# Performance work log

Measured on AMD Instinct MI355X. Metric: run time of the kernel, lower is better.

Reference implementation:

```python
import jax, jax.numpy as jnp
import numpy as np

N_IN = 200000
N_OUT = 600000
K = 27          # 3x3x3 kernel offsets
P = 150000      # kernel-map pairs per offset
C_IN = 96
C_OUT = 96
BN_EPS = 1e-5


def setup_inputs() -> dict:
    key = jax.random.key(0)
    k1, k2, k3, k4 = jax.random.split(key, 4)
    feats = jax.random.normal(k1, (N_IN, C_IN), dtype=jnp.float32)
    # kernel map: per offset, input-site indices and output-site indices
    in_idx = jax.random.randint(k2, (K, P), 0, N_IN, dtype=jnp.int32)
    out_idx = jax.random.randint(k3, (K, P), 0, N_OUT, dtype=jnp.int32)
    weight = jax.random.normal(k4, (K, C_IN, C_OUT), dtype=jnp.float32) * (1.0 / np.sqrt(C_IN * K))
    gamma = jnp.ones((C_OUT,), dtype=jnp.float32)
    beta = jnp.zeros((C_OUT,), dtype=jnp.float32)
    return {"feats": feats, "in_idx": in_idx, "out_idx": out_idx,
            "weight": weight, "gamma": gamma, "beta": beta}


def reference(feats, in_idx, out_idx, weight, gamma, beta):
    # Sparse transposed conv: gather -> matmul -> scatter-add per kernel offset.
    out = jnp.zeros((N_OUT, C_OUT), dtype=feats.dtype)
    for k in range(K):  # fixed small loop over kernel offsets (structurally distinct weights)
        contrib = feats[in_idx[k]] @ weight[k]          # [P, C_OUT]
        out = out.at[out_idx[k]].add(contrib)
    # BatchNorm (training-mode batch stats over active output sites), per channel
    mean = jnp.mean(out, axis=0)
    var = jnp.mean((out - mean) ** 2, axis=0)
    y = (out - mean) * jax.lax.rsqrt(var + BN_EPS) * gamma + beta
    # ReLU
    return jax.nn.relu(y)
```

## Files before the change

### kernel.cpp

```cpp
#include <hip/hip_runtime.h>
#include <hip/hip_bf16.h>

#define N_IN   200000
#define N_OUT  600000
#define KOFF   27
#define PPAIR  150000
#define NPAIR  (KOFF * PPAIR)
#define C      96
#define BN_EPS 1e-5f

using bf16x8 = __attribute__((ext_vector_type(8))) __bf16;
using f32x4  = __attribute__((ext_vector_type(4))) float;
using u32x2  = __attribute__((ext_vector_type(2))) unsigned int;
using u32x4  = __attribute__((ext_vector_type(4))) unsigned int;

static __device__ __forceinline__ unsigned short f2b(float x) {
    __hip_bfloat16 h = __float2bfloat16(x);
    return *reinterpret_cast<unsigned short*>(&h);
}
static __device__ __forceinline__ float b_lo(unsigned int u) { return __uint_as_float(u << 16); }
static __device__ __forceinline__ float b_hi(unsigned int u) { return __uint_as_float(u & 0xffff0000u); }

__global__ void cvt_feats(const float* __restrict__ src, unsigned short* __restrict__ dst) {
    int t = blockIdx.x * 256 + threadIdx.x;
    const float4* s4 = (const float4*)src;
    float4 a = s4[2 * t], b = s4[2 * t + 1];
    union { unsigned short u[8]; uint4 v; } r;
    r.u[0] = f2b(a.x); r.u[1] = f2b(a.y); r.u[2] = f2b(a.z); r.u[3] = f2b(a.w);
    r.u[4] = f2b(b.x); r.u[5] = f2b(b.y); r.u[6] = f2b(b.z); r.u[7] = f2b(b.w);
    ((uint4*)dst)[t] = r.v;
}

__global__ void cvt_w(const float* __restrict__ w, unsigned short* __restrict__ wt) {
    int t = blockIdx.x * 256 + threadIdx.x;
    int k = t / 9216;
    int rem = t - k * 9216;
    int o = rem / 96;
    int i = rem - o * 96;
    wt[t] = f2b(w[k * 9216 + i * 96 + o]);
}

__global__ void k_hist(const int* __restrict__ out_idx, int* __restrict__ counts,
                       unsigned char* __restrict__ lrank) {
    int t = blockIdx.x * 256 + threadIdx.x;
    if (t < NPAIR) lrank[t] = (unsigned char)atomicAdd(&counts[out_idx[t]], 1);
}

__global__ void k_bsum(const int* __restrict__ counts, int* __restrict__ bsum) {
    __shared__ int ls[256];
    int b = blockIdx.x, t = threadIdx.x;
    int base = b * 1024 + t * 4;
    int s = 0;
#pragma unroll
    for (int j = 0; j < 4; j++) { int i = base + j; if (i < N_OUT) s += counts[i]; }
    ls[t] = s;
    __syncthreads();
    for (int off = 128; off > 0; off >>= 1) {
        if (t < off) ls[t] += ls[t + off];
        __syncthreads();
    }
    if (t == 0) bsum[b] = ls[0];
}

__global__ void k_scan_bsum(const int* __restrict__ bsum, int* __restrict__ bsum_ex) {
    __shared__ int sc[1024];
    int t = threadIdx.x;
    int v = (t < 586) ? bsum[t] : 0;
    sc[t] = v;
    __syncthreads();
    for (int off = 1; off < 1024; off <<= 1) {
        int add = (t >= off) ? sc[t - off] : 0;
        __syncthreads();
        sc[t] += add;
        __syncthreads();
    }
    bsum_ex[t] = sc[t] - v;
}

__global__ void k_scan_local(int* __restrict__ csr, const int* __restrict__ bsum_ex) {
    __shared__ int sc[256];
    int b = blockIdx.x, t = threadIdx.x;
    int base = b * 1024 + t * 4;
    int c[4];
    int s = 0;
#pragma unroll
    for (int j = 0; j < 4; j++) {
        int i = base + j;
        c[j] = (i < N_OUT) ? csr[i] : 0;
        s += c[j];
    }
    sc[t] = s;
    __syncthreads();
    for (int off = 1; off < 256; off <<= 1) {
        int add = (t >= off) ? sc[t - off] : 0;
        __syncthreads();
        sc[t] += add;
        __syncthreads();
    }
    int run = bsum_ex[b] + sc[t] - s;
#pragma unroll
    for (int j = 0; j < 4; j++) {
        int i = base + j;
        if (i < N_OUT) {
            csr[i] = run;
            run += c[j];
            if (i == N_OUT - 1) csr[N_OUT] = run;
        }
    }
}

__global__ void k_perm(const int* __restrict__ out_idx, const unsigned char* __restrict__ lrank,
                       const int* __restrict__ csr, int* __restrict__ perm) {
    int t = blockIdx.x * 256 + threadIdx.x;
    if (t < NPAIR) perm[csr[out_idx[t]] + (int)lrank[t]] = t;
}

__global__ __launch_bounds__(256, 8) void contrib_k(
    const unsigned short* __restrict__ fb,
    const unsigned short* __restrict__ wt,
    const int* __restrict__ in_idx,
    unsigned short* __restrict__ contrib)
{
    __shared__ __align__(16) unsigned int lds[4][768];

    const int t    = threadIdx.x;
    const int k    = blockIdx.y;
    const int row0 = blockIdx.x * 64;
    const long kp  = (long)k * PPAIR;

    const int wave = t >> 6, lane = t & 63;
    const int quad = lane >> 4, l16 = lane & 15;

    const int pb = row0 + wave * 16 + l16;
    const int pc = (pb < PPAIR) ? pb : (PPAIR - 1);
    const int g  = in_idx[kp + pc];

    const unsigned short* arow  = fb + (size_t)g * 96 + quad * 8;
    const unsigned short* bbase = wt + (size_t)k * 9216 + l16 * 96 + quad * 8;

    f32x4 acc[6];
#pragma unroll
    for (int n = 0; n < 6; n++) acc[n] = (f32x4){0.f, 0.f, 0.f, 0.f};

#pragma unroll
    for (int kk = 0; kk < 3; kk++) {
        bf16x8 a = *(const bf16x8*)(arow + kk * 32);
#pragma unroll
        for (int n = 0; n < 6; n++) {
            bf16x8 b = *(const bf16x8*)(bbase + n * 16 * 96 + kk * 32);
            acc[n] = __builtin_amdgcn_mfma_f32_16x16x32_bf16(b, a, acc[n], 0, 0, 0);
        }
    }

#pragma unroll
    for (int n = 0; n < 6; n++) {
        u32x2 v;
        v.x = (unsigned)f2b(acc[n][0]) | ((unsigned)f2b(acc[n][1]) << 16);
        v.y = (unsigned)f2b(acc[n][2]) | ((unsigned)f2b(acc[n][3]) << 16);
        *(u32x2*)&lds[wave][l16 * 48 + n * 8 + quad * 2] = v;
    }
    __syncthreads();

    const int tile_row0 = row0 + wave * 16;
    if (tile_row0 + 16 <= PPAIR) {
        u32x4* cbase = (u32x4*)contrib;
        const size_t tb = (size_t)(kp + tile_row0) * 12;
#pragma unroll
        for (int s = 0; s < 3; s++) {
            u32x4 v = *(u32x4*)&lds[wave][s * 256 + lane * 4];
            __builtin_nontemporal_store(v, cbase + tb + s * 64 + lane);
        }
    }
}

__global__ __launch_bounds__(384) void reduce_bn(
    const unsigned short* __restrict__ contrib,
    const int* __restrict__ csr,
    const int* __restrict__ perm,
    float* __restrict__ out,
    float* __restrict__ sums)
{
    __shared__ float lsum[96], lq[96];
    int t = threadIdx.x;
    int rl = t / 24, c4 = t - rl * 24;
    float ps0 = 0.f, ps1 = 0.f, ps2 = 0.f, ps3 = 0.f;
    float pq0 = 0.f, pq1 = 0.f, pq2 = 0.f, pq3 = 0.f;

    for (int rb = blockIdx.x * 16; rb < N_OUT; rb += gridDim.x * 16) {
        int r = rb + rl;
        int s = csr[r], e = csr[r + 1];
        float a0 = 0.f, a1 = 0.f, a2 = 0.f, a3 = 0.f;
        int j = s;
        for (; j + 1 < e; j += 2) {
            int p0 = perm[j], p1 = perm[j + 1];
            uint2 u = *(const uint2*)(contrib + (size_t)p0 * 96 + c4 * 4);
            uint2 v = *(const uint2*)(contrib + (size_t)p1 * 96 + c4 * 4);
            a0 += b_lo(u.x); a1 += b_hi(u.x); a2 += b_lo(u.y); a3 += b_hi(u.y);
            a0 += b_lo(v.x); a1 += b_hi(v.x); a2 += b_lo(v.y); a3 += b_hi(v.y);
        }
        if (j < e) {
            int p0 = perm[j];
            uint2 u = *(const uint2*)(contrib + (size_t)p0 * 96 + c4 * 4);
            a0 += b_lo(u.x); a1 += b_hi(u.x); a2 += b_lo(u.y); a3 += b_hi(u.y);
        }
        *(float4*)(out + (size_t)r * 96 + c4 * 4) = make_float4(a0, a1, a2, a3);
        ps0 += a0; ps1 += a1; ps2 += a2; ps3 += a3;
        pq0 += a0 * a0; pq1 += a1 * a1; pq2 += a2 * a2; pq3 += a3 * a3;
    }

    if (t < 96) { lsum[t] = 0.f; lq[t] = 0.f; }
    __syncthreads();
    atomicAdd(&lsum[c4 * 4 + 0], ps0); atomicAdd(&lsum[c4 * 4 + 1], ps1);
    atomicAdd(&lsum[c4 * 4 + 2], ps2); atomicAdd(&lsum[c4 * 4 + 3], ps3);
    atomicAdd(&lq[c4 * 4 + 0], pq0);   atomicAdd(&lq[c4 * 4 + 1], pq1);
    atomicAdd(&lq[c4 * 4 + 2], pq2);   atomicAdd(&lq[c4 * 4 + 3], pq3);
    __syncthreads();
    if (t < 96) {
        atomicAdd(&sums[t], lsum[t]);
        atomicAdd(&sums[96 + t], lq[t]);
    }
}

__global__ void bn_final(float* __restrict__ sums, const float* __restrict__ gamma,
                         const float* __restrict__ beta) {
    int c = threadIdx.x;
    if (c < 96) {
        float mean = sums[c] * (1.0f / (float)N_OUT);
        float var  = sums[96 + c] * (1.0f / (float)N_OUT) - mean * mean;
        float inv  = rsqrtf(var + BN_EPS);
        float sc   = inv * gamma[c];
        sums[c]      = sc;
        sums[96 + c] = beta[c] - mean * sc;
    }
}

__global__ void bn_apply(float* __restrict__ out, const float* __restrict__ sums) {
    int t = blockIdx.x * 256 + threadIdx.x;
    int g = t % 24;
    float sc0 = sums[g * 4 + 0], sc1 = sums[g * 4 + 1];
    float sc2 = sums[g * 4 + 2], sc3 = sums[g * 4 + 3];
    float sh0 = sums[96 + g * 4 + 0], sh1 = sums[96 + g * 4 + 1];
    float sh2 = sums[96 + g * 4 + 2], sh3 = sums[96 + g * 4 + 3];
    f32x4* o4 = (f32x4*)out;
    for (long f = t; f < 14400000L; f += 258048) {
        f32x4 v = __builtin_nontemporal_load(o4 + f);
        v.x = fmaxf(v.x * sc0 + sh0, 0.f);
        v.y = fmaxf(v.y * sc1 + sh1, 0.f);
        v.z = fmaxf(v.z * sc2 + sh2, 0.f);
        v.w = fmaxf(v.w * sc3 + sh3, 0.f);
        __builtin_nontemporal_store(v, o4 + f);
    }
}

extern "C" void kernel_launch(void* const* d_in, const int* in_sizes, int n_in,
                              void* d_out, int out_size, void* d_ws, size_t ws_size,
                              hipStream_t stream) {
    const float* feats  = (const float*)d_in[0];
    const int* in_idx   = (const int*)d_in[1];
    const int* out_idx  = (const int*)d_in[2];
    const float* weight = (const float*)d_in[3];
    const float* gamma  = (const float*)d_in[4];
    const float* beta   = (const float*)d_in[5];
    float* out = (float*)d_out;

    char* ws = (char*)d_ws;
    size_t off = 0;
    unsigned short* fb      = (unsigned short*)(ws + off); off += 38400000;
    unsigned short* wt      = (unsigned short*)(ws + off); off += 497664;
    unsigned short* contrib = (unsigned short*)(ws + off); off += (size_t)NPAIR * 96 * 2;
    int* csr                = (int*)(ws + off); off += 2400016;
    int* bsum               = (int*)(ws + off); off += 4096;
    int* bsum_ex            = (int*)(ws + off); off += 4096;
    unsigned char* lrank    = (unsigned char*)(ws + off); off += NPAIR;
    int* perm               = (int*)(ws + off); off += (size_t)NPAIR * 4;
    float* sums             = (float*)(ws + off); off += 768;

    hipMemsetAsync(csr, 0, (size_t)N_OUT * sizeof(int), stream);
    hipMemsetAsync(sums, 0, 192 * sizeof(float), stream);

    cvt_feats<<<9375, 256, 0, stream>>>(feats, fb);
    cvt_w<<<972, 256, 0, stream>>>(weight, wt);

    k_hist<<<(NPAIR + 255) / 256, 256, 0, stream>>>(out_idx, csr, lrank);
    k_bsum<<<586, 256, 0, stream>>>(csr, bsum);
    k_scan_bsum<<<1, 1024, 0, stream>>>(bsum, bsum_ex);
    k_scan_local<<<586, 256, 0, stream>>>(csr, bsum_ex);
    k_perm<<<(NPAIR + 255) / 256, 256, 0, stream>>>(out_idx, lrank, csr, perm);

    contrib_k<<<dim3(2344, KOFF), 256, 0, stream>>>(fb, wt, in_idx, contrib);

    reduce_bn<<<9375, 384, 0, stream>>>(contrib, csr, perm, out, sums);
    bn_final<<<1, 128, 0, stream>>>(sums, gamma, beta);
    bn_apply<<<1008, 256, 0, stream>>>(out, sums);
}
```

Baseline: 1.458 ms.

## Stage gathered contrib rows in LDS with 16-byte cooperative loads in reduce_bn

The reduce kernel now loads each 16-row group's contiguous CSR pair range in chunks of 128 pairs. The whole block gathers those contrib rows into shared memory with 16-byte vector loads, replacing per-thread 8-byte gathers. Each row thread then sums its segment from LDS. This aims to widen memory transactions and raise bytes in flight for the gather. In exchange it adds several block-wide barriers per group and about 25KB of LDS per block, which lowers occupancy. The grid is also reduced to 2500 persistent-style blocks.

After: 1.308 ms. -10.3%, faster.

```diff
diff --git a/kernel.cpp b/kernel.cpp
--- a/kernel.cpp
+++ b/kernel.cpp
@@ -173,6 +173,7 @@
     }
 }
 
+#define RB_CHUNK 128
 __global__ __launch_bounds__(384) void reduce_bn(
     const unsigned short* __restrict__ contrib,
     const int* __restrict__ csr,
@@ -180,32 +181,63 @@
     float* __restrict__ out,
     float* __restrict__ sums)
 {
+    __shared__ __align__(16) unsigned short stage[RB_CHUNK * 96];
+    __shared__ int   lperm[RB_CHUNK];
+    __shared__ int   lcsr[17];
     __shared__ float lsum[96], lq[96];
-    int t = threadIdx.x;
-    int rl = t / 24, c4 = t - rl * 24;
+
+    const int t  = threadIdx.x;
+    const int rl = t / 24, c4 = t - rl * 24;
+
     float ps0 = 0.f, ps1 = 0.f, ps2 = 0.f, ps3 = 0.f;
     float pq0 = 0.f, pq1 = 0.f, pq2 = 0.f, pq3 = 0.f;
 
-    for (int rb = blockIdx.x * 16; rb < N_OUT; rb += gridDim.x * 16) {
-        int r = rb + rl;
-        int s = csr[r], e = csr[r + 1];
+    for (int grp = blockIdx.x; grp < N_OUT / 16; grp += gridDim.x) {
+        const int rb = grp * 16;
+        if (t < 17) lcsr[t] = csr[rb + t];
+        __syncthreads();
+        const int s0 = lcsr[0], s1 = lcsr[16];
+        const int rs = lcsr[rl], re = lcsr[rl + 1];
+
         float a0 = 0.f, a1 = 0.f, a2 = 0.f, a3 = 0.f;
-        int j = s;
-        for (; j + 1 < e; j += 2) {
-            int p0 = perm[j], p1 = perm[j + 1];
-            uint2 u = *(const uint2*)(contrib + (size_t)p0 * 96 + c4 * 4);
-            uint2 v = *(const uint2*)(contrib + (size_t)p1 * 96 + c4 * 4);
-            a0 += b_lo(u.x); a1 += b_hi(u.x); a2 += b_lo(u.y); a3 += b_hi(u.y);
-            a0 += b_lo(v.x); a1 += b_hi(v.x); a2 += b_lo(v.y); a3 += b_hi(v.y);
+
+        for (int cs = s0; cs < s1; cs += RB_CHUNK) {
+            const int ce  = (cs + RB_CHUNK < s1) ? cs + RB_CHUNK : s1;
+            const int n12 = (ce - cs) * 12;
+
+            if (t < RB_CHUNK) lperm[t] = (cs + t < s1) ? perm[cs + t] : 0;
+            __syncthreads();
+
+            const int i0 = t, i1 = t + 384, i2 = t + 768, i3 = t + 1152;
+            const bool g0 = i0 < n12, g1 = i1 < n12, g2 = i2 < n12, g3 = i3 < n12;
+            u32x4 v0, v1, v2, v3;
+            if (g0) { int e = i0 / 12, s = i0 - (i0 / 12) * 12;
+                      v0 = *(const u32x4*)(contrib + (size_t)lperm[e] * 96 + s * 8); }
+            if (g1) { int e = i1 / 12, s = i1 - (i1 / 12) * 12;
+                      v1 = *(const u32x4*)(contrib + (size_t)lperm[e] * 96 + s * 8); }
+            if (g2) { int e = i2 / 12, s = i2 - (i2 / 12) * 12;
+                      v2 = *(const u32x4*)(contrib + (size_t)lperm[e] * 96 + s * 8); }
+            if (g3) { int e = i3 / 12, s = i3 - (i3 / 12) * 12;
+                      v3 = *(const u32x4*)(contrib + (size_t)lperm[e] * 96 + s * 8); }
+            if (g0) *(u32x4*)&stage[i0 * 8] = v0;
+            if (g1) *(u32x4*)&stage[i1 * 8] = v1;
+            if (g2) *(u32x4*)&stage[i2 * 8] = v2;
+            if (g3) *(u32x4*)&stage[i3 * 8] = v3;
+            __syncthreads();
+
+            const int jb = (rs > cs) ? rs : cs;
+            const int je = (re < ce) ? re : ce;
+            for (int j = jb; j < je; j++) {
+                const unsigned short* sp = stage + (size_t)(j - cs) * 96 + c4 * 4;
+                uint2 u = *(const uint2*)sp;
+                a0 += b_lo(u.x); a1 += b_hi(u.x); a2 += b_lo(u.y); a3 += b_hi(u.y);
+            }
         }
-        if (j < e) {
-            int p0 = perm[j];
-            uint2 u = *(const uint2*)(contrib + (size_t)p0 * 96 + c4 * 4);
-            a0 += b_lo(u.x); a1 += b_hi(u.x); a2 += b_lo(u.y); a3 += b_hi(u.y);
-        }
-        *(float4*)(out + (size_t)r * 96 + c4 * 4) = make_float4(a0, a1, a2, a3);
+
+        *(float4*)(out + (size_t)(rb + rl) * 96 + c4 * 4) = make_float4(a0, a1, a2, a3);
         ps0 += a0; ps1 += a1; ps2 += a2; ps3 += a3;
         pq0 += a0 * a0; pq1 += a1 * a1; pq2 += a2 * a2; pq3 += a3 * a3;
+        __syncthreads();
     }
 
     if (t < 96) { lsum[t] = 0.f; lq[t] = 0.f; }
@@ -289,7 +321,7 @@
 
     contrib_k<<<dim3(2344, KOFF), 256, 0, stream>>>(fb, wt, in_idx, contrib);
 
-    reduce_bn<<<9375, 384, 0, stream>>>(contrib, csr, perm, out, sums);
+    reduce_bn<<<2500, 384, 0, stream>>>(contrib, csr, perm, out, sums);
     bn_final<<<1, 128, 0, stream>>>(sums, gamma, beta);
     bn_apply<<<1008, 256, 0, stream>>>(out, sums);
 }
```
